# Optimization experiments

Measured on AMD Instinct MI355X. Metric: run time of the kernel, lower is better.

Reference implementation:

```python
import jax, jax.numpy as jnp
import jax.scipy as jsp
import numpy as np

NUM_EMBEDDINGS = 256
EMBEDDING_DIM = 64
SPARSITY_LEVEL = 4
N_BINS = 16
COEF_MAX = 3.0
COEF_MU = 50.0
COMMITMENT_COST = 0.25
EPSILON = 1e-10


def _normalize_dict(dictionary):
    # F.normalize(dict, p=2, dim=0, eps): x / max(||x||_2, eps) per column
    nrm = jnp.linalg.norm(dictionary, axis=0, keepdims=True)
    return dictionary / jnp.maximum(nrm, EPSILON)


def _quantize_coeff_mu_law(coeff):
    inv_log1p_mu = 1.0 / np.log1p(COEF_MU)  # scalar constant
    c = jnp.clip(coeff, -COEF_MAX, COEF_MAX) / COEF_MAX
    encoded = jnp.sign(c) * jnp.log1p(jnp.abs(c) * COEF_MU) * inv_log1p_mu
    scaled = (encoded + 1.0) * ((N_BINS - 1) / 2.0)
    bin_idx = jnp.clip(jnp.round(scaled).astype(jnp.int32), 0, N_BINS - 1)
    # dequantize
    z = bin_idx.astype(coeff.dtype) * (2.0 / (N_BINS - 1)) - 1.0
    decoded = jnp.sign(z) * (jnp.expm1(jnp.abs(z) / inv_log1p_mu) / COEF_MU) * COEF_MAX
    return bin_idx, decoded


def batch_omp_with_support(X, Dn, K):
    # X: [M, Bs] signals, Dn: [M, N] normalized dictionary
    G = Dn.T @ Dn                       # [N, N] Gram
    h_bar = (Dn.T @ X).T                # [Bs, N] correlations
    Bs, N = h_bar.shape
    dt = h_bar.dtype
    h = h_bar
    mask = jnp.zeros((Bs, N), dtype=bool)
    L = jnp.ones((Bs, 1, 1), dtype=dt)  # incremental Cholesky of G[I, I]
    I = jnp.zeros((Bs, 0), dtype=jnp.int32)
    x_sel = jnp.zeros((Bs, 0), dtype=dt)
    rows = jnp.arange(Bs)
    for k in range(1, K + 1):  # K is small & static -> unrolled
        idx = jnp.argmax(jnp.abs(h) * (~mask), axis=1).astype(jnp.int32)
        mask = mask.at[rows, idx].set(True)
        if k > 1:
            G_stack = G[I, idx[:, None]]                     # [Bs, k-1]
            w = jsp.linalg.solve_triangular(L, G_stack[..., None], lower=True)  # [Bs,k-1,1]
            wT = jnp.swapaxes(w, 1, 2)                       # [Bs,1,k-1]
            w_corner = jnp.sqrt(jnp.clip(1.0 - jnp.sum(wT * wT, axis=2, keepdims=True), 1e-12))
            top = jnp.concatenate([L, jnp.zeros((Bs, k - 1, 1), dt)], axis=2)
            bot = jnp.concatenate([wT, w_corner], axis=2)
            L = jnp.concatenate([top, bot], axis=1)          # [Bs,k,k]
        I = jnp.concatenate([I, idx[:, None]], axis=1)       # [Bs,k]
        h_stack = jnp.take_along_axis(h_bar, I, axis=1)[..., None]  # [Bs,k,1]
        # cholesky_solve: L L^T x = h
        y = jsp.linalg.solve_triangular(L, h_stack, lower=True)
        xs = jsp.linalg.solve_triangular(jnp.swapaxes(L, 1, 2), y, lower=False)
        x_sel = xs[..., 0]                                   # [Bs,k] coeffs aligned w/ support
        beta = jnp.einsum('bk,bkn->bn', x_sel, G[I])         # [Bs,N]
        h = h_bar - beta
    return I, x_sel


def setup_inputs() -> dict:
    key = jax.random.key(0)
    k1, k2 = jax.random.split(key)
    z_e = jax.random.normal(k1, (32, EMBEDDING_DIM, 64, 64), dtype=jnp.float32)
    dictionary = jax.random.normal(k2, (EMBEDDING_DIM, NUM_EMBEDDINGS), dtype=jnp.float32) * 0.02
    return {"z_e": z_e, "dictionary": dictionary}


def reference(z_e, dictionary):
    B, C, H, W = z_e.shape
    Dn = _normalize_dict(dictionary)
    signals = jnp.transpose(z_e, (0, 2, 3, 1)).reshape(-1, C).T  # [C, B*H*W]
    # OMP runs with no grad (torch.no_grad in original)
    support, coeffs = jax.lax.stop_gradient(
        batch_omp_with_support(jax.lax.stop_gradient(signals), jax.lax.stop_gradient(Dn), SPARSITY_LEVEL)
    )
    # mu-law quantize coefficients (constants w.r.t. grads)
    bin_idx, coeffs_q = _quantize_coeff_mu_law(coeffs)
    # reconstruct with quantized coeffs; dictionary path is differentiable
    atoms = Dn.T[support]                                    # [Bs, K, C]
    recon_flat = jnp.einsum('bkc,bk->bc', atoms, coeffs_q)
    recon = jnp.transpose(recon_flat.reshape(B, H, W, C), (0, 3, 1, 2))
    # VQ-VAE style losses + STE
    e_latent_loss = jnp.mean((jax.lax.stop_gradient(recon) - z_e) ** 2)
    q_latent_loss = jnp.mean((recon - jax.lax.stop_gradient(z_e)) ** 2)
    loss = q_latent_loss + COMMITMENT_COST * e_latent_loss
    z_q = z_e + jax.lax.stop_gradient(recon - z_e)
    return z_q, loss


if __name__ == '__main__':
    out = reference(**setup_inputs())
    print(out[0].shape, out[1])
```

## Files before the change

### kernel.cpp

```cpp
#include <hip/hip_runtime.h>
#include <math.h>

#define NEMB 256
#define DIM 64
#define SIGS 128
#define THREADS 512
#define NSIG 131072
#define GRID (NSIG / SIGS)

#define LOG1P50 3.9318256327243257
#define INV_MU_F ((float)(1.0 / LOG1P50))
#define TWO15_F ((float)(2.0 / 15.0))

#define LB_SIG   0
#define LB_XS    32768
#define LB_QI    34816
#define LB_RED   36864
#define LDS_BYTES 36928

#define DPP_MAX(v, ctrl, rmask)  do {                                          \
    int _vi = __float_as_int(v);                                               \
    int _ti = __builtin_amdgcn_update_dpp(_vi, _vi, (ctrl), (rmask), 0xf, false);\
    (v) = fmaxf((v), __int_as_float(_ti));                                     \
} while (0)

static __device__ __forceinline__ float rl_f(float v, int lane)
{ return __int_as_float(__builtin_amdgcn_readlane(__float_as_int(v), lane)); }

__global__ void k_normalize(const float* __restrict__ D, float* __restrict__ Dn,
                            double* __restrict__ loss_acc)
{
#pragma clang fp contract(off)
    extern __shared__ float ds[];
    int tid = threadIdx.x;
    const float4* s4 = (const float4*)D;
    float4* d4 = (float4*)ds;
#pragma unroll
    for (int i = 0; i < 16; i++) d4[i * 256 + tid] = s4[i * 256 + tid];
    if (tid == 0) *loss_acc = 0.0;
    __syncthreads();
    float ss = 0.0f;
    for (int c = 0; c < DIM; c++) {
        float v = ds[c * NEMB + tid];
        float sq = v * v;
        ss = ss + sq;
    }
    float nrm = fmaxf(sqrtf(ss), 1e-10f);
    for (int c = 0; c < DIM; c++)
        Dn[c * NEMB + tid] = ds[c * NEMB + tid] / nrm;
}

__global__ void k_gram(const float* __restrict__ Dn, float* __restrict__ G)
{
    __shared__ float coli[DIM];
    int i = blockIdx.x, j = threadIdx.x;
    if (j < DIM) coli[j] = Dn[j * NEMB + i];
    __syncthreads();
    float s = 0.0f;
#pragma unroll
    for (int c = 0; c < DIM; c++) s = fmaf(coli[c], Dn[c * NEMB + j], s);
    G[i * NEMB + j] = s;
}

__device__ __forceinline__ float quant_decode(float coeff)
{
#pragma clang fp contract(off)
    float c = fminf(fmaxf(coeff, -3.0f), 3.0f) / 3.0f;
    float ac = fabsf(c);
    float sgn = (c > 0.0f) ? 1.0f : ((c < 0.0f) ? -1.0f : 0.0f);
    float l = log1pf(ac * 50.0f);
    float enc = (sgn * l) * INV_MU_F;
    float scaled = (enc + 1.0f) * 7.5f;
    int bin = (int)rintf(scaled);
    bin = bin < 0 ? 0 : (bin > 15 ? 15 : bin);
    float t = (float)bin * TWO15_F;
    float zv = t - 1.0f;
    float az = fabsf(zv);
    float sz = (zv > 0.0f) ? 1.0f : ((zv < 0.0f) ? -1.0f : 0.0f);
    float e = expm1f(az / INV_MU_F);
    return (sz * (e / 50.0f)) * 3.0f;
}

__launch_bounds__(THREADS, 6)
__global__ void k_omp(const float* __restrict__ z,
                      const float* __restrict__ Dn_g,
                      const float* __restrict__ G,
                      double* __restrict__ loss_acc,
                      float* __restrict__ zq)
{
    extern __shared__ char smem[];
    float* sig = (float*)(smem + LB_SIG);
    float* xsv = (float*)(smem + LB_XS);
    int* qi = (int*)(smem + LB_QI);
    double* red = (double*)(smem + LB_RED);

    int tid = threadIdx.x;
    int lane = tid & 63;
    int wid = tid >> 6;

    long sbase = (long)blockIdx.x * SIGS;
    int b = (int)(sbase >> 12);
    int pl0 = (int)(sbase & 4095);
    const float* zb = z + ((size_t)b << 18) + pl0;
    {
        int w = tid & (SIGS - 1);
        int g = tid >> 7;
#pragma unroll
        for (int i = 0; i < 16; i++) {
            int c = g * 16 + i;
            sig[c * SIGS + w] = zb[(size_t)c * 4096 + w];
        }
    }
    __syncthreads();

    for (int g2 = 0; g2 < 2; g2++) {
        int s0 = wid * 16 + g2 * 8;
        float hb[8][4];
#pragma unroll
        for (int a = 0; a < 8; a++)
#pragma unroll
            for (int t = 0; t < 4; t++) hb[a][t] = 0.0f;
#pragma unroll 8
        for (int c = 0; c < DIM; c++) {
            float4 sva = *(const float4*)(sig + c * SIGS + s0);
            float4 svb = *(const float4*)(sig + c * SIGS + s0 + 4);
            float s8[8] = {sva.x, sva.y, sva.z, sva.w, svb.x, svb.y, svb.z, svb.w};
            float4 dv = *(const float4*)(Dn_g + c * NEMB + 4 * lane);
            float d4[4] = {dv.x, dv.y, dv.z, dv.w};
#pragma unroll
            for (int a = 0; a < 8; a++) {
                hb[a][0] = fmaf(s8[a], d4[0], hb[a][0]);
                hb[a][1] = fmaf(s8[a], d4[1], hb[a][1]);
                hb[a][2] = fmaf(s8[a], d4[2], hb[a][2]);
                hb[a][3] = fmaf(s8[a], d4[3], hb[a][3]);
            }
        }

        {
#pragma clang fp contract(off)
            unsigned m4 = 0;
            float Lm[4][4];
            float y[4], xs[4];
            int vIv[4] = {0, 0, 0, 0};
            int vidx = 0;
            float vhsel = 0.0f;
            int IvS[8][4];
            Lm[0][0] = 1.0f; Lm[1][1] = 1.0f; Lm[2][2] = 1.0f; Lm[3][3] = 1.0f;

#pragma unroll
            for (int kk = 0; kk < 4; kk++) {
                float sxs[3][8];
                if (kk > 0) {
#pragma unroll
                    for (int a = 0; a < 8; a++)
#pragma unroll
                        for (int jj = 0; jj < 3; jj++)
                            if (jj < kk) sxs[jj][a] = rl_f(xs[jj], a);
                }
#pragma unroll
                for (int a = 0; a < 8; a++) {
                    float h[4];
                    if (kk == 0) {
                        h[0] = hb[a][0]; h[1] = hb[a][1]; h[2] = hb[a][2]; h[3] = hb[a][3];
                    } else {
                        float gr[3][4];
#pragma unroll
                        for (int jj = 0; jj < 3; jj++)
                            if (jj < kk) {
                                const float4 gv = *(const float4*)(G + (size_t)IvS[a][jj] * NEMB + 4 * lane);
                                gr[jj][0] = gv.x; gr[jj][1] = gv.y; gr[jj][2] = gv.z; gr[jj][3] = gv.w;
                            }
#pragma unroll
                        for (int j = 0; j < 4; j++) {
                            float bsum = 0.0f;
#pragma unroll
                            for (int jj = 0; jj < 3; jj++)
                                if (jj < kk) { float p = sxs[jj][a] * gr[jj][j]; bsum = bsum + p; }
                            h[j] = hb[a][j] - bsum;
                        }
                    }
                    float bv = -1.0f;
                    int bj = 0;
#pragma unroll
                    for (int j = 0; j < 4; j++) {
                        float v = (m4 & (1u << (4 * a + j))) ? 0.0f : fabsf(h[j]);
                        if (v > bv) { bv = v; bj = j; }
                    }
                    float rd = bv;
                    DPP_MAX(rd, 0x111, 0xf);
                    DPP_MAX(rd, 0x112, 0xf);
                    DPP_MAX(rd, 0x114, 0xf);
                    DPP_MAX(rd, 0x118, 0xf);
                    DPP_MAX(rd, 0x142, 0xa);
                    DPP_MAX(rd, 0x143, 0xc);
                    float vmax = rl_f(rd, 63);
                    unsigned long long mball = __ballot(bv == vmax);
                    int owner = __ffsll(mball) - 1;
                    int idx = __builtin_amdgcn_readlane(4 * lane + bj, owner);
                    if (lane == owner) m4 |= (1u << (4 * a + bj));
                    float hbsel = (bj == 0) ? hb[a][0] : ((bj == 1) ? hb[a][1] : ((bj == 2) ? hb[a][2] : hb[a][3]));
                    float hs = rl_f(hbsel, owner);
                    bool isa = (lane == a);
                    vidx = isa ? idx : vidx;
                    vhsel = isa ? hs : vhsel;
                    vIv[kk] = isa ? idx : vIv[kk];
                    IvS[a][kk] = idx;
                }
                if (kk > 0) {
                    float Gs[3], w[3];
#pragma unroll
                    for (int jj = 0; jj < 3; jj++)
                        if (jj < kk) Gs[jj] = G[(unsigned)(vIv[jj] * NEMB + vidx)];
#pragma unroll
                    for (int r = 0; r < 3; r++) {
                        if (r < kk) {
                            float acc = 0.0f;
#pragma unroll
                            for (int cc = 0; cc < 3; cc++)
                                if (cc < r) { float p = Lm[r][cc] * w[cc]; acc = acc + p; }
                            float t2 = Gs[r] - acc;
                            w[r] = t2 / Lm[r][r];
                        }
                    }
                    float ssum = 0.0f;
#pragma unroll
                    for (int jj = 0; jj < 3; jj++)
                        if (jj < kk) { float p = w[jj] * w[jj]; ssum = ssum + p; }
                    float om = 1.0f - ssum;
                    float wc = sqrtf(fmaxf(om, 1e-12f));
#pragma unroll
                    for (int cc = 0; cc < 3; cc++)
                        if (cc < kk) Lm[kk][cc] = w[cc];
                    Lm[kk][kk] = wc;
                }
                {
                    float acc = 0.0f;
#pragma unroll
                    for (int cc = 0; cc < 3; cc++)
                        if (cc < kk) { float p = Lm[kk][cc] * y[cc]; acc = acc + p; }
                    float t2 = vhsel - acc;
                    y[kk] = t2 / Lm[kk][kk];
                }
#pragma unroll
                for (int r = 3; r >= 0; r--) {
                    if (r <= kk) {
                        float acc = 0.0f;
#pragma unroll
                        for (int cc = 0; cc < 4; cc++)
                            if (cc > r && cc <= kk) { float p = Lm[cc][r] * xs[cc]; acc = acc + p; }
                        float t2 = y[r] - acc;
                        xs[r] = t2 / Lm[r][r];
                    }
                }
            }
            if (lane < 8) {
                int s = s0 + lane;
#pragma unroll
                for (int j = 0; j < 4; j++) {
                    xsv[j * SIGS + s] = xs[j];
                    qi[j * SIGS + s] = vIv[j];
                }
            }
        }
    }
    __syncthreads();

    {
        int jq = tid >> 7;
        int wq = tid & (SIGS - 1);
        xsv[jq * SIGS + wq] = quant_decode(xsv[jq * SIGS + wq]);
    }
    __syncthreads();

    double lsum = 0.0;
    float* zqb = zq + ((size_t)b << 18) + pl0;
    {
#pragma clang fp contract(off)
        int w = tid & (SIGS - 1);
        int g = tid >> 7;
        float q0 = xsv[0 * SIGS + w], q1 = xsv[1 * SIGS + w];
        float q2 = xsv[2 * SIGS + w], q3 = xsv[3 * SIGS + w];
        int i0 = qi[0 * SIGS + w], i1 = qi[1 * SIGS + w];
        int i2 = qi[2 * SIGS + w], i3 = qi[3 * SIGS + w];
#pragma unroll
        for (int ci = 0; ci < 16; ci++) {
            int c = g * 16 + ci;
            const float* dr = Dn_g + c * NEMB;
            float p0 = q0 * dr[i0];
            float p1 = q1 * dr[i1];
            float p2 = q2 * dr[i2];
            float p3 = q3 * dr[i3];
            float r = p0 + p1;
            r = r + p2;
            r = r + p3;
            float zev = sig[c * SIGS + w];
            float d = r - zev;
            float zqv = zev + d;
            lsum += (double)d * (double)d;
            zqb[(size_t)c * 4096 + w] = zqv;
        }
    }
#pragma unroll
    for (int off = 32; off > 0; off >>= 1) lsum += __shfl_xor(lsum, off);
    if (lane == 0) red[wid] = lsum;
    __syncthreads();
    if (tid == 0) {
        double t = 0.0;
#pragma unroll
        for (int i = 0; i < 8; i++) t += red[i];
        atomicAdd(loss_acc, t);
    }
}

__global__ void k_final(const double* __restrict__ loss_acc, float* __restrict__ out)
{
    double m = loss_acc[0] / 8388608.0;
    out[0] = (float)(m + 0.25 * m);
}

extern "C" void kernel_launch(void* const* d_in, const int* in_sizes, int n_in,
                              void* d_out, int out_size, void* d_ws, size_t ws_size,
                              hipStream_t stream)
{
    const float* z = (const float*)d_in[0];
    const float* D = (const float*)d_in[1];
    float* out = (float*)d_out;
    char* ws = (char*)d_ws;
    double* loss_acc = (double*)ws;
    float* Dn = (float*)(ws + 256);
    float* G = (float*)(ws + 256 + 65536);

    (void)hipFuncSetAttribute(reinterpret_cast<const void*>(k_normalize),
                              hipFuncAttributeMaxDynamicSharedMemorySize, 65536);
    k_normalize<<<1, NEMB, 65536, stream>>>(D, Dn, loss_acc);
    k_gram<<<NEMB, NEMB, 0, stream>>>(Dn, G);
    (void)hipFuncSetAttribute(reinterpret_cast<const void*>(k_omp),
                              hipFuncAttributeMaxDynamicSharedMemorySize, LDS_BYTES);
    k_omp<<<GRID, THREADS, LDS_BYTES, stream>>>(z, Dn, G, loss_acc, out);
    k_final<<<1, 1, 0, stream>>>(loss_acc, out + 8388608);
    (void)in_sizes; (void)n_in; (void)out_size; (void)ws_size;
}
```

Baseline: 304.7 us.

## Fuse normalize+Gram kernels, fold final loss into OMP, process 16 signals per wave

Merges dictionary normalization and Gram computation into one kernel where each block renormalizes in LDS and computes one Gram row. The final loss kernel is removed by having the last OMP block, detected with an atomic counter, write the loss. Each wavefront now handles all 16 of its signals in one pass with a 64-bit mask, lowering launch bounds to 4 waves per SIMD. This cuts launches and loop overhead but raises register pressure and lowers occupancy.

Result: slower. 336.3 us (+10.4%).

```diff
diff --git a/kernel.cpp b/kernel.cpp
--- a/kernel.cpp
+++ b/kernel.cpp
@@ -27,17 +27,19 @@
 static __device__ __forceinline__ float rl_f(float v, int lane)
 { return __int_as_float(__builtin_amdgcn_readlane(__float_as_int(v), lane)); }
 
-__global__ void k_normalize(const float* __restrict__ D, float* __restrict__ Dn,
-                            double* __restrict__ loss_acc)
+__global__ void k_ng(const float* __restrict__ D, float* __restrict__ Dn,
+                     float* __restrict__ G, double* __restrict__ loss_acc,
+                     unsigned* __restrict__ cnt)
 {
 #pragma clang fp contract(off)
     extern __shared__ float ds[];
     int tid = threadIdx.x;
+    int i = blockIdx.x;
     const float4* s4 = (const float4*)D;
     float4* d4 = (float4*)ds;
 #pragma unroll
-    for (int i = 0; i < 16; i++) d4[i * 256 + tid] = s4[i * 256 + tid];
-    if (tid == 0) *loss_acc = 0.0;
+    for (int k = 0; k < 16; k++) d4[k * 256 + tid] = s4[k * 256 + tid];
+    if (i == 0 && tid == 0) { *loss_acc = 0.0; *cnt = 0u; }
     __syncthreads();
     float ss = 0.0f;
     for (int c = 0; c < DIM; c++) {
@@ -47,19 +49,14 @@
     }
     float nrm = fmaxf(sqrtf(ss), 1e-10f);
     for (int c = 0; c < DIM; c++)
-        Dn[c * NEMB + tid] = ds[c * NEMB + tid] / nrm;
-}
-
-__global__ void k_gram(const float* __restrict__ Dn, float* __restrict__ G)
-{
-    __shared__ float coli[DIM];
-    int i = blockIdx.x, j = threadIdx.x;
-    if (j < DIM) coli[j] = Dn[j * NEMB + i];
-    __syncthreads();
+        ds[c * NEMB + tid] = ds[c * NEMB + tid] / nrm;
+    __syncthreads();
+    if (i < DIM) Dn[i * NEMB + tid] = ds[i * NEMB + tid];
     float s = 0.0f;
 #pragma unroll
-    for (int c = 0; c < DIM; c++) s = fmaf(coli[c], Dn[c * NEMB + j], s);
-    G[i * NEMB + j] = s;
+    for (int c = 0; c < DIM; c++)
+        s = fmaf(ds[c * NEMB + i], ds[c * NEMB + tid], s);
+    G[i * NEMB + tid] = s;
 }
 
 __device__ __forceinline__ float quant_decode(float coeff)
@@ -81,11 +78,12 @@
     return (sz * (e / 50.0f)) * 3.0f;
 }
 
-__launch_bounds__(THREADS, 6)
+__launch_bounds__(THREADS, 4)
 __global__ void k_omp(const float* __restrict__ z,
                       const float* __restrict__ Dn_g,
                       const float* __restrict__ G,
                       double* __restrict__ loss_acc,
+                      unsigned* __restrict__ cnt,
                       float* __restrict__ zq)
 {
     extern __shared__ char smem[];
@@ -113,60 +111,57 @@
     }
     __syncthreads();
 
-    for (int g2 = 0; g2 < 2; g2++) {
-        int s0 = wid * 16 + g2 * 8;
-        float hb[8][4];
-#pragma unroll
-        for (int a = 0; a < 8; a++)
+    {
+        int s0 = wid * 16;
+        float hb[16][4];
+#pragma unroll
+        for (int a = 0; a < 16; a++)
 #pragma unroll
             for (int t = 0; t < 4; t++) hb[a][t] = 0.0f;
-#pragma unroll 8
+#pragma unroll 4
         for (int c = 0; c < DIM; c++) {
             float4 sva = *(const float4*)(sig + c * SIGS + s0);
             float4 svb = *(const float4*)(sig + c * SIGS + s0 + 4);
-            float s8[8] = {sva.x, sva.y, sva.z, sva.w, svb.x, svb.y, svb.z, svb.w};
+            float4 svc = *(const float4*)(sig + c * SIGS + s0 + 8);
+            float4 svd = *(const float4*)(sig + c * SIGS + s0 + 12);
+            float s16[16] = {sva.x, sva.y, sva.z, sva.w, svb.x, svb.y, svb.z, svb.w,
+                             svc.x, svc.y, svc.z, svc.w, svd.x, svd.y, svd.z, svd.w};
             float4 dv = *(const float4*)(Dn_g + c * NEMB + 4 * lane);
             float d4[4] = {dv.x, dv.y, dv.z, dv.w};
 #pragma unroll
-            for (int a = 0; a < 8; a++) {
-                hb[a][0] = fmaf(s8[a], d4[0], hb[a][0]);
-                hb[a][1] = fmaf(s8[a], d4[1], hb[a][1]);
-                hb[a][2] = fmaf(s8[a], d4[2], hb[a][2]);
-                hb[a][3] = fmaf(s8[a], d4[3], hb[a][3]);
+            for (int a = 0; a < 16; a++) {
+                hb[a][0] = fmaf(s16[a], d4[0], hb[a][0]);
+                hb[a][1] = fmaf(s16[a], d4[1], hb[a][1]);
+                hb[a][2] = fmaf(s16[a], d4[2], hb[a][2]);
+                hb[a][3] = fmaf(s16[a], d4[3], hb[a][3]);
             }
         }
 
         {
 #pragma clang fp contract(off)
-            unsigned m4 = 0;
+            unsigned long long m4 = 0ull;
             float Lm[4][4];
             float y[4], xs[4];
             int vIv[4] = {0, 0, 0, 0};
             int vidx = 0;
             float vhsel = 0.0f;
-            int IvS[8][4];
+            int IvS[16][4];
             Lm[0][0] = 1.0f; Lm[1][1] = 1.0f; Lm[2][2] = 1.0f; Lm[3][3] = 1.0f;
 
 #pragma unroll
             for (int kk = 0; kk < 4; kk++) {
-                float sxs[3][8];
-                if (kk > 0) {
-#pragma unroll
-                    for (int a = 0; a < 8; a++)
-#pragma unroll
-                        for (int jj = 0; jj < 3; jj++)
-                            if (jj < kk) sxs[jj][a] = rl_f(xs[jj], a);
-                }
-#pragma unroll
-                for (int a = 0; a < 8; a++) {
+#pragma unroll
+                for (int a = 0; a < 16; a++) {
                     float h[4];
                     if (kk == 0) {
                         h[0] = hb[a][0]; h[1] = hb[a][1]; h[2] = hb[a][2]; h[3] = hb[a][3];
                     } else {
                         float gr[3][4];
+                        float sxs[3];
 #pragma unroll
                         for (int jj = 0; jj < 3; jj++)
                             if (jj < kk) {
+                                sxs[jj] = rl_f(xs[jj], a);
                                 const float4 gv = *(const float4*)(G + (size_t)IvS[a][jj] * NEMB + 4 * lane);
                                 gr[jj][0] = gv.x; gr[jj][1] = gv.y; gr[jj][2] = gv.z; gr[jj][3] = gv.w;
                             }
@@ -175,7 +170,7 @@
                             float bsum = 0.0f;
 #pragma unroll
                             for (int jj = 0; jj < 3; jj++)
-                                if (jj < kk) { float p = sxs[jj][a] * gr[jj][j]; bsum = bsum + p; }
+                                if (jj < kk) { float p = sxs[jj] * gr[jj][j]; bsum = bsum + p; }
                             h[j] = hb[a][j] - bsum;
                         }
                     }
@@ -183,7 +178,7 @@
                     int bj = 0;
 #pragma unroll
                     for (int j = 0; j < 4; j++) {
-                        float v = (m4 & (1u << (4 * a + j))) ? 0.0f : fabsf(h[j]);
+                        float v = ((m4 >> (4 * a + j)) & 1ull) ? 0.0f : fabsf(h[j]);
                         if (v > bv) { bv = v; bj = j; }
                     }
                     float rd = bv;
@@ -197,7 +192,7 @@
                     unsigned long long mball = __ballot(bv == vmax);
                     int owner = __ffsll(mball) - 1;
                     int idx = __builtin_amdgcn_readlane(4 * lane + bj, owner);
-                    if (lane == owner) m4 |= (1u << (4 * a + bj));
+                    if (lane == owner) m4 |= (1ull << (4 * a + bj));
                     float hbsel = (bj == 0) ? hb[a][0] : ((bj == 1) ? hb[a][1] : ((bj == 2) ? hb[a][2] : hb[a][3]));
                     float hs = rl_f(hbsel, owner);
                     bool isa = (lane == a);
@@ -253,7 +248,7 @@
                     }
                 }
             }
-            if (lane < 8) {
+            if (lane < 16) {
                 int s = s0 + lane;
 #pragma unroll
                 for (int j = 0; j < 4; j++) {
@@ -309,13 +304,14 @@
 #pragma unroll
         for (int i = 0; i < 8; i++) t += red[i];
         atomicAdd(loss_acc, t);
-    }
-}
-
-__global__ void k_final(const double* __restrict__ loss_acc, float* __restrict__ out)
-{
-    double m = loss_acc[0] / 8388608.0;
-    out[0] = (float)(m + 0.25 * m);
+        __threadfence();
+        unsigned prev = atomicAdd(cnt, 1u);
+        if (prev == GRID - 1) {
+            double total = atomicAdd(loss_acc, 0.0);
+            double m = total / 8388608.0;
+            zq[8388608] = (float)(m + 0.25 * m);
+        }
+    }
 }
 
 extern "C" void kernel_launch(void* const* d_in, const int* in_sizes, int n_in,
@@ -327,16 +323,15 @@
     float* out = (float*)d_out;
     char* ws = (char*)d_ws;
     double* loss_acc = (double*)ws;
+    unsigned* cnt = (unsigned*)(ws + 8);
     float* Dn = (float*)(ws + 256);
     float* G = (float*)(ws + 256 + 65536);
 
-    (void)hipFuncSetAttribute(reinterpret_cast<const void*>(k_normalize),
+    (void)hipFuncSetAttribute(reinterpret_cast<const void*>(k_ng),
                               hipFuncAttributeMaxDynamicSharedMemorySize, 65536);
-    k_normalize<<<1, NEMB, 65536, stream>>>(D, Dn, loss_acc);
-    k_gram<<<NEMB, NEMB, 0, stream>>>(Dn, G);
+    k_ng<<<NEMB, NEMB, 65536, stream>>>(D, Dn, G, loss_acc, cnt);
     (void)hipFuncSetAttribute(reinterpret_cast<const void*>(k_omp),
                               hipFuncAttributeMaxDynamicSharedMemorySize, LDS_BYTES);
-    k_omp<<<GRID, THREADS, LDS_BYTES, stream>>>(z, Dn, G, loss_acc, out);
-    k_final<<<1, 1, 0, stream>>>(loss_acc, out + 8388608);
+    k_omp<<<GRID, THREADS, LDS_BYTES, stream>>>(z, Dn, G, loss_acc, cnt, out);
     (void)in_sizes; (void)n_in; (void)out_size; (void)ws_size;
 }
```
